# Optimization experiments

Hardware: AMD Instinct MI355X
Metric: run time of the kernel (lower is better)

## Reference

```python
import jax, jax.numpy as jnp
import numpy as np

N_NODES = 50000
N_EDGES = 500000
D_IN = 128
D_OUT = 128
BN_EPS = 1e-5


def setup_inputs() -> dict:
    key = jax.random.key(0)
    k0, k1, k2, k3, k4 = jax.random.split(key, 5)
    edge_attr = jax.random.normal(k0, (N_EDGES, D_IN), jnp.float32)
    node_attr = jax.random.normal(k1, (N_NODES, D_IN), jnp.float32)
    row = jax.random.randint(k2, (N_EDGES,), 0, N_NODES)  # senders
    col = jax.random.randint(k3, (N_EDGES,), 0, N_NODES)  # receivers
    W = jax.random.normal(k4, (D_OUT, 3 * D_IN), jnp.float32) / jnp.sqrt(3.0 * D_IN)
    b = jnp.zeros((D_OUT,), jnp.float32)
    gamma = jnp.ones((D_OUT,), jnp.float32)
    beta = jnp.zeros((D_OUT,), jnp.float32)
    return {"edge_attr": edge_attr, "node_attr": node_attr, "W": W, "b": b,
            "gamma": gamma, "beta": beta, "row": row, "col": col}


def reference(edge_attr, node_attr, W, b, gamma, beta, row, col):
    # scatter-sum edge features to receiver and sender nodes  [N_NODES, D_IN]
    recv = jax.ops.segment_sum(edge_attr, col, num_segments=N_NODES)
    send = jax.ops.segment_sum(edge_attr, row, num_segments=N_NODES)
    # concat(receivers_aggr, senders_aggr, node_attr)  [N_NODES, 3*D_IN]
    x = jnp.concatenate([recv, send, node_attr], axis=-1)
    # Linear projection + ReLU (dropout p=0.0 -> identity)
    h = jax.nn.relu(x @ W.T + b)
    # BatchNorm1d (training-mode batch stats, biased variance)
    mu = jnp.mean(h, axis=0)
    var = jnp.mean((h - mu) ** 2, axis=0)
    return gamma * (h - mu) * jax.lax.rsqrt(var + BN_EPS) + beta
```

## Files before the change

### kernel.cpp

```cpp
#include <hip/hip_runtime.h>
#include <hip/hip_bf16.h>

#define N_NODES 50000
#define N_EDGES 500000
#define D_IN    128
#define D_K     384
#define D_OUT   128
#define BN_EPS  1e-5f
#define N_TASK  (2 * N_NODES)
#define CAP     64
#define NBX     ((N_NODES + 255) / 256)
#define PSTRIDE 200

typedef __bf16 bf16x8 __attribute__((ext_vector_type(8)));
typedef __bf16 bf16x4 __attribute__((ext_vector_type(4)));
typedef float  f32x4  __attribute__((ext_vector_type(4)));

#define OFF_AGG   0ULL
#define OFF_CNT   25600000ULL
#define OFF_EID   26000000ULL
#define OFF_PSTAT 51600000ULL
#define OFF_SCALE 51804800ULL
#define OFF_SHIFT 51805312ULL
#define OFF_HB    51805824ULL

__global__ __launch_bounds__(256) void bucket_kernel(const int* __restrict__ row,
                                                     const int* __restrict__ col,
                                                     int* __restrict__ cnt,
                                                     int* __restrict__ eid) {
    int i = blockIdx.x * blockDim.x + threadIdx.x;
    if (i < N_EDGES) {
        const int c = col[i];
        const int r = atomicAdd(&cnt[c], 1);
        if (r < CAP) eid[(size_t)c * CAP + r] = i;
        const int rw = row[i];
        const int r2 = atomicAdd(&cnt[N_NODES + rw], 1);
        if (r2 < CAP) eid[((size_t)N_NODES + rw) * CAP + r2] = i;
    }
}

__global__ __launch_bounds__(256) void gather_kernel(const float* __restrict__ edge_attr,
                                                     const int* __restrict__ cnt,
                                                     const int* __restrict__ eid,
                                                     __bf16* __restrict__ agg) {
    const int hl  = threadIdx.x & 31;
    const int hwv = (threadIdx.x >> 5) & 1;
    const int wid = blockIdx.x * 8 + (threadIdx.x >> 5);
    const int n   = min(cnt[wid], CAP);
    const size_t beg = (size_t)wid * CAP;
    const int c   = hl * 4;
    f32x4 acc0 = (f32x4)0.0f, acc1 = (f32x4)0.0f;

    const int e_reg = (hl < n) ? eid[beg + hl] : 0;
#pragma unroll
    for (int j = 0; j < 32; ++j) {
        const int e = __shfl(e_reg, hwv * 32 + j);
        if (j < n) {
            const f32x4 v = *(const f32x4*)(edge_attr + (size_t)e * D_IN + c);
            if (j & 1) acc1 += v; else acc0 += v;
        }
    }
    if (__builtin_expect(n > 32, 0)) {
        for (int cb = 32; cb < n; cb += 32) {
            const int m2 = n - cb;
            const int e2 = (hl < m2) ? eid[beg + cb + hl] : 0;
#pragma unroll
            for (int j = 0; j < 32; ++j) {
                const int e = __shfl(e2, hwv * 32 + j);
                if (j < m2) {
                    const f32x4 v = *(const f32x4*)(edge_attr + (size_t)e * D_IN + c);
                    if (j & 1) acc1 += v; else acc0 += v;
                }
            }
        }
    }
    acc0 += acc1;

    bf16x4 o;
#pragma unroll
    for (int q = 0; q < 4; ++q) o[q] = (__bf16)acc0[q];
    *(bf16x4*)(agg + (size_t)wid * D_IN + c) = o;
}

#define ROW_B 768
__global__ __launch_bounds__(512) void gemm_kernel(
    const __bf16* __restrict__ agg, const float* __restrict__ node_attr,
    const float* __restrict__ W, const float* __restrict__ bias,
    __bf16* __restrict__ hb, float* __restrict__ pstat) {
    __shared__ __align__(16) char Ws[64 * ROW_B];
    __shared__ float sred[2][8][64];

    const int lane = threadIdx.x & 63;
    const int w    = threadIdx.x >> 6;
    const int m    = lane & 15;
    const int g    = lane >> 4;
    const int cy   = blockIdx.y;

    {
        const float* src = W + (size_t)cy * 64 * D_K;
#pragma unroll
        for (int i = 0; i < 6; ++i) {
            const int idx = i * 512 + threadIdx.x;
            const int r   = idx / 48;
            const int c8  = idx % 48;
            const float* p = src + (size_t)r * D_K + c8 * 8;
            f32x4 v0 = *(const f32x4*)p, v1 = *(const f32x4*)(p + 4);
            bf16x8 v;
#pragma unroll
            for (int q = 0; q < 4; ++q) { v[q] = (__bf16)v0[q]; v[q + 4] = (__bf16)v1[q]; }
            *(bf16x8*)(Ws + r * ROW_B + ((c8 * 16) ^ ((r & 7) << 4))) = v;
        }
    }
    __syncthreads();

    const int nodeA0 = blockIdx.x * 256 + w * 32 + m;
    const int nodeA1 = nodeA0 + 16;

    f32x4 acc[2][4];
#pragma unroll
    for (int i = 0; i < 2; ++i)
#pragma unroll
        for (int f = 0; f < 4; ++f) acc[i][f] = (f32x4)0.0f;

#pragma unroll
    for (int ks = 0; ks < 12; ++ks) {
        const int k0 = ks * 32;
        bf16x8 a0, a1;
#pragma unroll
        for (int i = 0; i < 8; ++i) { a0[i] = (__bf16)0.0f; a1[i] = (__bf16)0.0f; }
        if (ks < 8) {
            const size_t base = (size_t)(k0 >> 7) * (N_NODES * D_IN) + (k0 & 127) + g * 8;
            if (nodeA0 < N_NODES) a0 = *(const bf16x8*)(agg + base + (size_t)nodeA0 * D_IN);
            if (nodeA1 < N_NODES) a1 = *(const bf16x8*)(agg + base + (size_t)nodeA1 * D_IN);
        } else {
            const size_t base = (k0 - 256) + g * 8;
            if (nodeA0 < N_NODES) {
                const float* p = node_attr + (size_t)nodeA0 * D_IN + base;
                f32x4 v0 = *(const f32x4*)p, v1 = *(const f32x4*)(p + 4);
#pragma unroll
                for (int i = 0; i < 4; ++i) { a0[i] = (__bf16)v0[i]; a0[i + 4] = (__bf16)v1[i]; }
            }
            if (nodeA1 < N_NODES) {
                const float* p = node_attr + (size_t)nodeA1 * D_IN + base;
                f32x4 v0 = *(const f32x4*)p, v1 = *(const f32x4*)(p + 4);
#pragma unroll
                for (int i = 0; i < 4; ++i) { a1[i] = (__bf16)v0[i]; a1[i + 4] = (__bf16)v1[i]; }
            }
        }
#pragma unroll
        for (int f = 0; f < 4; ++f) {
            const int r = f * 16 + m;
            const int cb = (k0 + g * 8) * 2;
            bf16x8 bfrag = *(const bf16x8*)(Ws + r * ROW_B + (cb ^ ((r & 7) << 4)));
            acc[0][f] = __builtin_amdgcn_mfma_f32_16x16x32_bf16(a0, bfrag, acc[0][f], 0, 0, 0);
            acc[1][f] = __builtin_amdgcn_mfma_f32_16x16x32_bf16(a1, bfrag, acc[1][f], 0, 0, 0);
        }
    }

#pragma unroll
    for (int f = 0; f < 4; ++f) {
        const int j  = cy * 64 + f * 16 + m;
        const float bj = bias[j];
        float s1 = 0.0f, s2 = 0.0f;
#pragma unroll
        for (int i = 0; i < 2; ++i) {
#pragma unroll
            for (int r = 0; r < 4; ++r) {
                const int nodeC = blockIdx.x * 256 + w * 32 + i * 16 + g * 4 + r;
                float v = acc[i][f][r] + bj;
                v = v > 0.0f ? v : 0.0f;
                if (nodeC < N_NODES) {
                    hb[(size_t)nodeC * D_OUT + j] = (__bf16)v;
                    s1 += v;
                    s2 += v * v;
                }
            }
        }
        s1 += __shfl_xor(s1, 16, 64);  s2 += __shfl_xor(s2, 16, 64);
        s1 += __shfl_xor(s1, 32, 64);  s2 += __shfl_xor(s2, 32, 64);
        if (lane < 16) { sred[0][w][f * 16 + m] = s1; sred[1][w][f * 16 + m] = s2; }
    }
    __syncthreads();
    if (threadIdx.x < 128) {
        const int s = threadIdx.x >> 6;
        const int c = threadIdx.x & 63;
        float v = 0.0f;
#pragma unroll
        for (int q = 0; q < 8; ++q) v += sred[s][q][c];
        pstat[(size_t)(s * 128 + cy * 64 + c) * PSTRIDE + blockIdx.x] = v;
    }
}

__global__ __launch_bounds__(256) void bn_finalize_kernel(
    const float* __restrict__ pstat, const float* __restrict__ gamma,
    const float* __restrict__ beta, float* __restrict__ scale, float* __restrict__ shift) {
    const int j = blockIdx.x;
    float a1 = 0.0f, a2 = 0.0f;
    for (int b = threadIdx.x; b < NBX; b += 256) {
        a1 += pstat[(size_t)j * PSTRIDE + b];
        a2 += pstat[(size_t)(128 + j) * PSTRIDE + b];
    }
#pragma unroll
    for (int ofs = 32; ofs >= 1; ofs >>= 1) {
        a1 += __shfl_xor(a1, ofs, 64);
        a2 += __shfl_xor(a2, ofs, 64);
    }
    __shared__ float w1[4], w2[4];
    if ((threadIdx.x & 63) == 0) { w1[threadIdx.x >> 6] = a1; w2[threadIdx.x >> 6] = a2; }
    __syncthreads();
    if (threadIdx.x == 0) {
        const float S1 = w1[0] + w1[1] + w1[2] + w1[3];
        const float S2 = w2[0] + w2[1] + w2[2] + w2[3];
        const float inv_n = 1.0f / (float)N_NODES;
        const float mu  = S1 * inv_n;
        const float var = S2 * inv_n - mu * mu;
        const float sc  = gamma[j] * rsqrtf(var + BN_EPS);
        scale[j] = sc;
        shift[j] = beta[j] - mu * sc;
    }
}

__global__ __launch_bounds__(256) void bn_apply_kernel(
    const __bf16* __restrict__ hb, float* __restrict__ out,
    const float* __restrict__ scale, const float* __restrict__ shift) {
    size_t i = ((size_t)blockIdx.x * blockDim.x + threadIdx.x) * 8;
    if (i >= (size_t)N_NODES * D_OUT) return;
    const int j0 = (int)(i & 127);
    bf16x8 v = *(const bf16x8*)(hb + i);
    f32x4 a, b;
#pragma unroll
    for (int q = 0; q < 4; ++q) {
        a[q] = (float)v[q]     * scale[j0 + q]     + shift[j0 + q];
        b[q] = (float)v[q + 4] * scale[j0 + 4 + q] + shift[j0 + 4 + q];
    }
    *(f32x4*)(out + i)     = a;
    *(f32x4*)(out + i + 4) = b;
}

extern "C" void kernel_launch(void* const* d_in, const int* in_sizes, int n_in,
                              void* d_out, int out_size, void* d_ws, size_t ws_size,
                              hipStream_t stream) {
    const float* edge_attr = (const float*)d_in[0];
    const float* node_attr = (const float*)d_in[1];
    const float* W         = (const float*)d_in[2];
    const float* bias      = (const float*)d_in[3];
    const float* gamma     = (const float*)d_in[4];
    const float* beta      = (const float*)d_in[5];
    const int*   row       = (const int*)d_in[6];
    const int*   col       = (const int*)d_in[7];
    float* out = (float*)d_out;

    char* ws = (char*)d_ws;
    __bf16* agg   = (__bf16*)(ws + OFF_AGG);
    int*    cnt   = (int*)(ws + OFF_CNT);
    int*    eid   = (int*)(ws + OFF_EID);
    float*  pstat = (float*)(ws + OFF_PSTAT);
    float*  scale = (float*)(ws + OFF_SCALE);
    float*  shift = (float*)(ws + OFF_SHIFT);
    __bf16* hb    = (__bf16*)(ws + OFF_HB);

    hipMemsetAsync(cnt, 0, N_TASK * sizeof(int), stream);

    bucket_kernel<<<(N_EDGES + 255) / 256, 256, 0, stream>>>(row, col, cnt, eid);
    gather_kernel<<<N_TASK / 8, 256, 0, stream>>>(edge_attr, cnt, eid, agg);
    dim3 ggrid(NBX, 2);
    gemm_kernel<<<ggrid, 512, 0, stream>>>(agg, node_attr, W, bias, hb, pstat);
    bn_finalize_kernel<<<128, 256, 0, stream>>>(pstat, gamma, beta, scale, shift);
    bn_apply_kernel<<<(N_NODES * D_OUT / 8 + 255) / 256, 256, 0, stream>>>(hb, out, scale, shift);
}
```

Baseline: 210.7 us.

## Stage gathered edge rows through LDS via global_load_lds in gather kernel

The gather kernel now uses one full wavefront per node task instead of a half-wave, and issues direct global-to-LDS 16-byte loads for up to 16 edge rows per batch. It waits on all loads, then sums the rows from shared memory with 2 floats per lane. The goal is more memory-level parallelism, with many loads in flight before any accumulation. In exchange it needs a full vmcnt(0) drain per batch, uses LDS, and halves the work per lane, which may reduce the overlap the earlier register-accumulating loop had.

```diff
diff --git a/kernel.cpp b/kernel.cpp
--- a/kernel.cpp
+++ b/kernel.cpp
@@ -14,7 +14,9 @@
 
 typedef __bf16 bf16x8 __attribute__((ext_vector_type(8)));
 typedef __bf16 bf16x4 __attribute__((ext_vector_type(4)));
+typedef __bf16 bf16x2 __attribute__((ext_vector_type(2)));
 typedef float  f32x4  __attribute__((ext_vector_type(4)));
+typedef float  f32x2  __attribute__((ext_vector_type(2)));
 
 #define OFF_AGG   0ULL
 #define OFF_CNT   25600000ULL
@@ -23,6 +25,12 @@
 #define OFF_SCALE 51804800ULL
 #define OFF_SHIFT 51805312ULL
 #define OFF_HB    51805824ULL
+
+__device__ __forceinline__ void gload_lds16(const void* g, void* l) {
+    __builtin_amdgcn_global_load_lds(
+        (const __attribute__((address_space(1))) void*)g,
+        (__attribute__((address_space(3))) void*)l, 16, 0, 0);
+}
 
 __global__ __launch_bounds__(256) void bucket_kernel(const int* __restrict__ row,
                                                      const int* __restrict__ col,
@@ -43,43 +51,38 @@
                                                      const int* __restrict__ cnt,
                                                      const int* __restrict__ eid,
                                                      __bf16* __restrict__ agg) {
-    const int hl  = threadIdx.x & 31;
-    const int hwv = (threadIdx.x >> 5) & 1;
-    const int wid = blockIdx.x * 8 + (threadIdx.x >> 5);
-    const int n   = min(cnt[wid], CAP);
+    __shared__ __align__(16) float ebuf[4][16][D_IN];
+    const int lane = threadIdx.x & 63;
+    const int w    = threadIdx.x >> 6;
+    const int wid  = blockIdx.x * 4 + w;
+    const int n    = __builtin_amdgcn_readfirstlane(min(cnt[wid], CAP));
     const size_t beg = (size_t)wid * CAP;
-    const int c   = hl * 4;
-    f32x4 acc0 = (f32x4)0.0f, acc1 = (f32x4)0.0f;
-
-    const int e_reg = (hl < n) ? eid[beg + hl] : 0;
-#pragma unroll
-    for (int j = 0; j < 32; ++j) {
-        const int e = __shfl(e_reg, hwv * 32 + j);
-        if (j < n) {
-            const f32x4 v = *(const f32x4*)(edge_attr + (size_t)e * D_IN + c);
-            if (j & 1) acc1 += v; else acc0 += v;
-        }
-    }
-    if (__builtin_expect(n > 32, 0)) {
-        for (int cb = 32; cb < n; cb += 32) {
-            const int m2 = n - cb;
-            const int e2 = (hl < m2) ? eid[beg + cb + hl] : 0;
-#pragma unroll
-            for (int j = 0; j < 32; ++j) {
-                const int e = __shfl(e2, hwv * 32 + j);
-                if (j < m2) {
-                    const f32x4 v = *(const f32x4*)(edge_attr + (size_t)e * D_IN + c);
-                    if (j & 1) acc1 += v; else acc0 += v;
-                }
-            }
+    const int half = lane >> 5;
+    const int hl   = lane & 31;
+    f32x2 acc0 = (f32x2)0.0f, acc1 = (f32x2)0.0f;
+
+    for (int cb = 0; cb < n; cb += 16) {
+        const int m2 = min(n - cb, 16);
+        const int kp = (m2 + 1) >> 1;
+        const int e_reg = (lane < m2) ? eid[beg + cb + lane] : 0;
+        for (int k = 0; k < kp; ++k) {
+            const int e = __shfl(e_reg, 2 * k + half);
+            gload_lds16(edge_attr + (size_t)e * D_IN + hl * 4, &ebuf[w][2 * k][0]);
+        }
+        asm volatile("s_waitcnt vmcnt(0)" ::: "memory");
+        __builtin_amdgcn_sched_barrier(0);
+#pragma unroll
+        for (int r = 0; r < 16; r += 2) {
+            if (r < m2)     acc0 += *(const f32x2*)&ebuf[w][r][lane * 2];
+            if (r + 1 < m2) acc1 += *(const f32x2*)&ebuf[w][r + 1][lane * 2];
         }
     }
     acc0 += acc1;
 
-    bf16x4 o;
-#pragma unroll
-    for (int q = 0; q < 4; ++q) o[q] = (__bf16)acc0[q];
-    *(bf16x4*)(agg + (size_t)wid * D_IN + c) = o;
+    bf16x2 o;
+    o[0] = (__bf16)acc0[0];
+    o[1] = (__bf16)acc0[1];
+    *(bf16x2*)(agg + (size_t)wid * D_IN + lane * 2) = o;
 }
 
 #define ROW_B 768
@@ -262,7 +265,7 @@
     hipMemsetAsync(cnt, 0, N_TASK * sizeof(int), stream);
 
     bucket_kernel<<<(N_EDGES + 255) / 256, 256, 0, stream>>>(row, col, cnt, eid);
-    gather_kernel<<<N_TASK / 8, 256, 0, stream>>>(edge_attr, cnt, eid, agg);
+    gather_kernel<<<N_TASK / 4, 256, 0, stream>>>(edge_attr, cnt, eid, agg);
     dim3 ggrid(NBX, 2);
     gemm_kernel<<<ggrid, 512, 0, stream>>>(agg, node_attr, W, bias, hb, pstat);
     bn_finalize_kernel<<<128, 256, 0, stream>>>(pstat, gamma, beta, scale, shift);
```

Result: slower. 217.4 us (+3.2%).

## Pre-convert edge features to bf16 and gather from bf16 copy with one wave per node

Applied to the files above, without the earlier changes.

A new prep kernel streams edge_attr once, converting it to a bf16 copy while also bucketing edges. The gather kernel then reads that half-size copy for its random per-edge gathers, and assigns one 64-lane wave per task, with the two halves handling alternate edges and combined by a cross-half shuffle. The aim is to shrink the random-access gather traffic, which is read twice (once per direction), at the cost of an extra full read and write pass over edge_attr and reduced input precision before summation.

```diff
diff --git a/kernel.cpp b/kernel.cpp
--- a/kernel.cpp
+++ b/kernel.cpp
@@ -11,6 +11,7 @@
 #define CAP     64
 #define NBX     ((N_NODES + 255) / 256)
 #define PSTRIDE 200
+#define NV8     ((N_EDGES * D_IN) / 8)
 
 typedef __bf16 bf16x8 __attribute__((ext_vector_type(8)));
 typedef __bf16 bf16x4 __attribute__((ext_vector_type(4)));
@@ -23,12 +24,23 @@
 #define OFF_SCALE 51804800ULL
 #define OFF_SHIFT 51805312ULL
 #define OFF_HB    51805824ULL
-
-__global__ __launch_bounds__(256) void bucket_kernel(const int* __restrict__ row,
-                                                     const int* __restrict__ col,
-                                                     int* __restrict__ cnt,
-                                                     int* __restrict__ eid) {
-    int i = blockIdx.x * blockDim.x + threadIdx.x;
+#define OFF_EBF   65000000ULL
+
+__global__ __launch_bounds__(256) void prep_kernel(const float* __restrict__ edge_attr,
+                                                   const int* __restrict__ row,
+                                                   const int* __restrict__ col,
+                                                   __bf16* __restrict__ ebf,
+                                                   int* __restrict__ cnt,
+                                                   int* __restrict__ eid) {
+    const int i = blockIdx.x * blockDim.x + threadIdx.x;
+    if (i < NV8) {
+        const float* p = edge_attr + (size_t)i * 8;
+        f32x4 a = *(const f32x4*)p, b = *(const f32x4*)(p + 4);
+        bf16x8 v;
+#pragma unroll
+        for (int q = 0; q < 4; ++q) { v[q] = (__bf16)a[q]; v[q + 4] = (__bf16)b[q]; }
+        *(bf16x8*)(ebf + (size_t)i * 8) = v;
+    }
     if (i < N_EDGES) {
         const int c = col[i];
         const int r = atomicAdd(&cnt[c], 1);
@@ -39,47 +51,48 @@
     }
 }
 
-__global__ __launch_bounds__(256) void gather_kernel(const float* __restrict__ edge_attr,
+__global__ __launch_bounds__(256) void gather_kernel(const __bf16* __restrict__ ebf,
                                                      const int* __restrict__ cnt,
                                                      const int* __restrict__ eid,
                                                      __bf16* __restrict__ agg) {
-    const int hl  = threadIdx.x & 31;
-    const int hwv = (threadIdx.x >> 5) & 1;
-    const int wid = blockIdx.x * 8 + (threadIdx.x >> 5);
-    const int n   = min(cnt[wid], CAP);
+    const int lane = threadIdx.x & 63;
+    const int w    = threadIdx.x >> 6;
+    const int wid  = blockIdx.x * 4 + w;
+    const int n    = __builtin_amdgcn_readfirstlane(min(cnt[wid], CAP));
     const size_t beg = (size_t)wid * CAP;
-    const int c   = hl * 4;
+    const int half = lane >> 5;
+    const int hl   = lane & 31;
     f32x4 acc0 = (f32x4)0.0f, acc1 = (f32x4)0.0f;
 
-    const int e_reg = (hl < n) ? eid[beg + hl] : 0;
-#pragma unroll
-    for (int j = 0; j < 32; ++j) {
-        const int e = __shfl(e_reg, hwv * 32 + j);
-        if (j < n) {
-            const f32x4 v = *(const f32x4*)(edge_attr + (size_t)e * D_IN + c);
-            if (j & 1) acc1 += v; else acc0 += v;
-        }
-    }
-    if (__builtin_expect(n > 32, 0)) {
-        for (int cb = 32; cb < n; cb += 32) {
-            const int m2 = n - cb;
-            const int e2 = (hl < m2) ? eid[beg + cb + hl] : 0;
-#pragma unroll
-            for (int j = 0; j < 32; ++j) {
-                const int e = __shfl(e2, hwv * 32 + j);
-                if (j < m2) {
-                    const f32x4 v = *(const f32x4*)(edge_attr + (size_t)e * D_IN + c);
-                    if (j & 1) acc1 += v; else acc0 += v;
-                }
-            }
+    const int e_reg = (lane < n) ? eid[beg + lane] : 0;
+    int j = 0;
+    for (; j + 4 <= n; j += 4) {
+        const int ea = __shfl(e_reg, j + half);
+        const int eb = __shfl(e_reg, j + 2 + half);
+        const bf16x4 va = *(const bf16x4*)(ebf + (size_t)ea * D_IN + hl * 4);
+        const bf16x4 vb = *(const bf16x4*)(ebf + (size_t)eb * D_IN + hl * 4);
+#pragma unroll
+        for (int q = 0; q < 4; ++q) { acc0[q] += (float)va[q]; acc1[q] += (float)vb[q]; }
+    }
+    for (; j < n; j += 2) {
+        const int e = __shfl(e_reg, j + half);
+        if (j + half < n) {
+            const bf16x4 v = *(const bf16x4*)(ebf + (size_t)e * D_IN + hl * 4);
+#pragma unroll
+            for (int q = 0; q < 4; ++q) acc0[q] += (float)v[q];
         }
     }
     acc0 += acc1;
 
-    bf16x4 o;
-#pragma unroll
-    for (int q = 0; q < 4; ++q) o[q] = (__bf16)acc0[q];
-    *(bf16x4*)(agg + (size_t)wid * D_IN + c) = o;
+#pragma unroll
+    for (int q = 0; q < 4; ++q) acc0[q] += __shfl_xor(acc0[q], 32);
+
+    if (lane < 32) {
+        bf16x4 o;
+#pragma unroll
+        for (int q = 0; q < 4; ++q) o[q] = (__bf16)acc0[q];
+        *(bf16x4*)(agg + (size_t)wid * D_IN + hl * 4) = o;
+    }
 }
 
 #define ROW_B 768
@@ -258,11 +271,12 @@
     float*  scale = (float*)(ws + OFF_SCALE);
     float*  shift = (float*)(ws + OFF_SHIFT);
     __bf16* hb    = (__bf16*)(ws + OFF_HB);
+    __bf16* ebf   = (__bf16*)(ws + OFF_EBF);
 
     hipMemsetAsync(cnt, 0, N_TASK * sizeof(int), stream);
 
-    bucket_kernel<<<(N_EDGES + 255) / 256, 256, 0, stream>>>(row, col, cnt, eid);
-    gather_kernel<<<N_TASK / 8, 256, 0, stream>>>(edge_attr, cnt, eid, agg);
+    prep_kernel<<<(NV8 + 255) / 256, 256, 0, stream>>>(edge_attr, row, col, ebf, cnt, eid);
+    gather_kernel<<<N_TASK / 4, 256, 0, stream>>>(ebf, cnt, eid, agg);
     dim3 ggrid(NBX, 2);
     gemm_kernel<<<ggrid, 512, 0, stream>>>(agg, node_attr, W, bias, hb, pstat);
     bn_finalize_kernel<<<128, 256, 0, stream>>>(pstat, gamma, beta, scale, shift);
```

Result: slower. 227.9 us (+8.2%).
